# Kernel optimization log

Measured on AMD Instinct MI355X. Metric: run time of the kernel, lower is better.

The kernel has to match this reference:

```python
import jax, jax.numpy as jnp
import numpy as np
import math

B, N, D, H, A, OBS, NB = 256, 64, 512, 8, 64, 128, 4
HD = D // H
EPS = 1e-5


def layernorm(x, g, b):
    mu = jnp.mean(x, axis=-1, keepdims=True)
    var = jnp.mean((x - mu) ** 2, axis=-1, keepdims=True)
    return (x - mu) * jax.lax.rsqrt(var + EPS) * g + b


def gelu(x):
    return jax.nn.gelu(x, approximate=False)  # torch nn.GELU default = exact erf


def mha_masked(k_in, v_in, q_in, wq, wk, wv, wp, bq, bk, bv, bp):
    # weights stored [in, out]; torch Linear computes x @ W.T, same math with random init
    b, l, d = q_in.shape
    q = (q_in @ wq + bq).reshape(b, l, H, HD).transpose(0, 2, 1, 3)  # [B,H,L,hd]
    k = (k_in @ wk + bk).reshape(b, l, H, HD).transpose(0, 2, 1, 3)
    v = (v_in @ wv + bv).reshape(b, l, H, HD).transpose(0, 2, 1, 3)
    att = jnp.einsum('bhqd,bhkd->bhqk', q, k) * (1.0 / math.sqrt(HD))
    causal = jnp.tril(jnp.ones((l, l), dtype=bool))  # registered tril buffer in original MAT code
    att = jnp.where(causal[None, None], att, -jnp.inf)
    att = jax.nn.softmax(att, axis=-1)
    y = jnp.einsum('bhqk,bhkd->bhqd', att, v)
    y = y.transpose(0, 2, 1, 3).reshape(b, l, d)
    return y @ wp + bp


def setup_inputs() -> dict:
    key = jax.random.key(0)
    ks = iter(jax.random.split(key, 32))
    s = 0.02
    inp = {
        'action': jax.random.normal(next(ks), (B, N, A + 1), jnp.float32),
        'obs_rep': jax.random.normal(next(ks), (B, N, D), jnp.float32),
        'obs': jax.random.normal(next(ks), (B, N, OBS), jnp.float32),
        'w_ae': jax.random.normal(next(ks), (A + 1, D), jnp.float32) * s,
        'ln0_g': jnp.ones((D,), jnp.float32),
        'ln0_b': jnp.zeros((D,), jnp.float32),
        'blk_ln_g': jnp.ones((NB, 3, D), jnp.float32),
        'blk_ln_b': jnp.zeros((NB, 3, D), jnp.float32),
        'blk_wq': jax.random.normal(next(ks), (NB, 2, D, D), jnp.float32) * s,
        'blk_wk': jax.random.normal(next(ks), (NB, 2, D, D), jnp.float32) * s,
        'blk_wv': jax.random.normal(next(ks), (NB, 2, D, D), jnp.float32) * s,
        'blk_wp': jax.random.normal(next(ks), (NB, 2, D, D), jnp.float32) * s,
        'blk_bq': jnp.zeros((NB, 2, D), jnp.float32),
        'blk_bk': jnp.zeros((NB, 2, D), jnp.float32),
        'blk_bv': jnp.zeros((NB, 2, D), jnp.float32),
        'blk_bp': jnp.zeros((NB, 2, D), jnp.float32),
        'blk_w1': jax.random.normal(next(ks), (NB, D, D), jnp.float32) * s,
        'blk_b1': jnp.zeros((NB, D), jnp.float32),
        'blk_w2': jax.random.normal(next(ks), (NB, D, D), jnp.float32) * s,
        'blk_b2': jnp.zeros((NB, D), jnp.float32),
        'wh1': jax.random.normal(next(ks), (D, D), jnp.float32) * s,
        'bh1': jnp.zeros((D,), jnp.float32),
        'lnh_g': jnp.ones((D,), jnp.float32),
        'lnh_b': jnp.zeros((D,), jnp.float32),
        'wh2': jax.random.normal(next(ks), (D, A), jnp.float32) * s,
        'bh2': jnp.zeros((A,), jnp.float32),
    }
    return inp


def reference(action, obs_rep, obs, w_ae, ln0_g, ln0_b, blk_ln_g, blk_ln_b,
              blk_wq, blk_wk, blk_wv, blk_wp, blk_bq, blk_bk, blk_bv, blk_bp,
              blk_w1, blk_b1, blk_w2, blk_b2, wh1, bh1, lnh_g, lnh_b, wh2, bh2):
    # action encoder: Linear(no bias) + GELU, then LayerNorm
    x = layernorm(gelu(action @ w_ae), ln0_g, ln0_b)
    for i in range(NB):
        # sublayer 1: masked self-attn + residual + LN
        a1 = mha_masked(x, x, x, blk_wq[i, 0], blk_wk[i, 0], blk_wv[i, 0], blk_wp[i, 0],
                        blk_bq[i, 0], blk_bk[i, 0], blk_bv[i, 0], blk_bp[i, 0])
        x = layernorm(x + a1, blk_ln_g[i, 0], blk_ln_b[i, 0])
        # sublayer 2: masked cross-attn (key=x, value=x, query=obs_rep) + residual with obs_rep + LN
        a2 = mha_masked(x, x, obs_rep, blk_wq[i, 1], blk_wk[i, 1], blk_wv[i, 1], blk_wp[i, 1],
                        blk_bq[i, 1], blk_bk[i, 1], blk_bv[i, 1], blk_bp[i, 1])
        x = layernorm(obs_rep + a2, blk_ln_g[i, 1], blk_ln_b[i, 1])
        # sublayer 3: GELU MLP (D -> D -> D) + residual + LN
        m = gelu(x @ blk_w1[i] + blk_b1[i]) @ blk_w2[i] + blk_b2[i]
        x = layernorm(x + m, blk_ln_g[i, 2], blk_ln_b[i, 2])
    # head: Linear + GELU + LN + Linear
    h = layernorm(gelu(x @ wh1 + bh1), lnh_g, lnh_b)
    logit = h @ wh2 + bh2
    return logit
```

## Files before the change

kernel.cpp:

```cpp
#include <hip/hip_runtime.h>
#include <hip/hip_bf16.h>
#include <math.h>

namespace {

constexpr int B  = 256;
constexpr int N  = 64;
constexpr int D  = 512;
constexpr int H  = 8;
constexpr int NBLK = 4;
constexpr int M  = B * N;
constexpr float EPS = 1e-5f;
constexpr float SCALE = 0.125f;
constexpr int NEVER = 1 << 20;

typedef __attribute__((ext_vector_type(8))) short short8b;
typedef __attribute__((ext_vector_type(4))) float f32x4;

__device__ __forceinline__ float gelu_exact(float x) {
  return 0.5f * x * (1.0f + erff(x * 0.70710678118654752440f));
}

__device__ __forceinline__ unsigned short f2b_bits(float f) {
  __hip_bfloat16 h = __float2bfloat16(f);
  return *reinterpret_cast<unsigned short*>(&h);
}

#define GLOBAL_AS __attribute__((address_space(1)))
#define LDS_AS    __attribute__((address_space(3)))

__device__ __forceinline__ void gload_lds16(const void* g, void* l) {
  __builtin_amdgcn_global_load_lds((const GLOBAL_AS void*)g, (LDS_AS void*)l, 16, 0, 0);
}

template<bool GELU, int SPLIT>
__global__ __launch_bounds__(512, 2) void gemm_dp_kernel(
    const __hip_bfloat16* __restrict__ A,
    const __hip_bfloat16* __restrict__ Wt,
    const float* __restrict__ bias,
    __hip_bfloat16* __restrict__ out1, int ostr1,
    __hip_bfloat16* __restrict__ vt, int gy) {
  constexpr int K = 512;
  constexpr int NT = 8;
  __shared__ __hip_bfloat16 Als[3][128][64];
  __shared__ __hip_bfloat16 Bls[3][256][64];

  const int nwg = gridDim.x;
  const int hw  = blockIdx.x;
  const int cpx = nwg >> 3;
  const int lg  = (hw & 7) * cpx + (hw >> 3);
  const int bm  = (lg / gy) * 128;
  const int bn  = (lg % gy) * 256;

  const int tid  = threadIdx.x;
  const int wave = tid >> 6;
  const int lane = tid & 63;
  const int wm   = (wave >> 2) * 64;
  const int wn   = (wave & 3) * 64;
  const int fr   = lane & 15;
  const int fg   = lane >> 4;

  const int srow  = tid >> 3;
  const int sslot = (tid & 7) ^ (srow & 7);
  const __hip_bfloat16* gA = A  + (size_t)(bm + srow) * K + sslot * 8;
  const __hip_bfloat16* gB = Wt + (size_t)(bn + srow) * K + sslot * 8;

  auto STAGE = [&](int buf, int kt) {
    const int ko = kt * 64;
    char* la = (char*)&Als[buf][0][0] + wave * 1024;
    char* lb = (char*)&Bls[buf][0][0] + wave * 1024;
    gload_lds16(gA + ko,           la);
    gload_lds16(gA + 64 * K + ko,  la + 8192);
    gload_lds16(gB + ko,           lb);
    gload_lds16(gB + 64 * K + ko,  lb + 8192);
    gload_lds16(gB + 128 * K + ko, lb + 16384);
    gload_lds16(gB + 192 * K + ko, lb + 24576);
  };

  auto lda = [&](int buf, int mi, int ks) -> short8b {
    const int row  = wm + mi * 16 + fr;
    const int byte = row * 128 + (((ks << 2) | fg) ^ (fr & 7)) * 16;
    return *reinterpret_cast<const short8b*>((const char*)&Als[buf][0][0] + byte);
  };
  auto ldb = [&](int buf, int ni, int ks) -> short8b {
    const int row  = wn + ni * 16 + fr;
    const int byte = row * 128 + (((ks << 2) | fg) ^ (fr & 7)) * 16;
    return *reinterpret_cast<const short8b*>((const char*)&Bls[buf][0][0] + byte);
  };

  STAGE(0, 0);
  STAGE(1, 1);
  asm volatile("s_waitcnt vmcnt(6)" ::: "memory");
  __builtin_amdgcn_sched_barrier(0);
  __builtin_amdgcn_s_barrier();
  __builtin_amdgcn_sched_barrier(0);

  f32x4 acc[4][4] = {};
  for (int t = 0; t < NT; ++t) {
    const int cur = t % 3;
    if (t + 2 < NT) STAGE((t + 2) % 3, t + 2);

    short8b a0[4], b0[4], a1[4], b1[4];
#pragma unroll
    for (int mi = 0; mi < 4; ++mi) a0[mi] = lda(cur, mi, 0);
#pragma unroll
    for (int ni = 0; ni < 4; ++ni) b0[ni] = ldb(cur, ni, 0);
#pragma unroll
    for (int mi = 0; mi < 4; ++mi) a1[mi] = lda(cur, mi, 1);
#pragma unroll
    for (int ni = 0; ni < 4; ++ni) b1[ni] = ldb(cur, ni, 1);

    __builtin_amdgcn_s_setprio(1);
#pragma unroll
    for (int mi = 0; mi < 4; ++mi)
#pragma unroll
      for (int ni = 0; ni < 4; ++ni)
        acc[mi][ni] = __builtin_amdgcn_mfma_f32_16x16x32_bf16(a0[mi], b0[ni], acc[mi][ni], 0, 0, 0);
#pragma unroll
    for (int mi = 0; mi < 4; ++mi)
#pragma unroll
      for (int ni = 0; ni < 4; ++ni)
        acc[mi][ni] = __builtin_amdgcn_mfma_f32_16x16x32_bf16(a1[mi], b1[ni], acc[mi][ni], 0, 0, 0);
    __builtin_amdgcn_s_setprio(0);

    if (t + 2 < NT) {
      asm volatile("s_waitcnt vmcnt(6)" ::: "memory");
    } else {
      asm volatile("s_waitcnt vmcnt(0)" ::: "memory");
    }
    __builtin_amdgcn_sched_barrier(0);
    __builtin_amdgcn_s_barrier();
    __builtin_amdgcn_sched_barrier(0);
  }

#pragma unroll
  for (int ni = 0; ni < 4; ++ni) {
    const int col = bn + wn + ni * 16 + fr;
    const float bv = bias ? bias[col] : 0.f;
#pragma unroll
    for (int mi = 0; mi < 4; ++mi) {
      const int row0 = bm + wm + mi * 16 + fg * 4;
      if (col >= SPLIT) {
        const int vcol = col - SPLIT;
        ushort4 o;
        o.x = f2b_bits(acc[mi][ni][0] + bv);
        o.y = f2b_bits(acc[mi][ni][1] + bv);
        o.z = f2b_bits(acc[mi][ni][2] + bv);
        o.w = f2b_bits(acc[mi][ni][3] + bv);
        const int b8 = row0 >> 6, nl = row0 & 63;
        const int hh = vcol >> 6, dl = vcol & 63;
        *reinterpret_cast<ushort4*>(vt +
            ((size_t)(b8 * 8 + hh) * 4096 + dl * 64 + nl)) = o;
      } else {
#pragma unroll
        for (int q = 0; q < 4; ++q) {
          float v = acc[mi][ni][q] + bv;
          if (GELU) v = gelu_exact(v);
          out1[(size_t)(row0 + q) * ostr1 + col] = __float2bfloat16(v);
        }
      }
    }
  }
}

template<int KSTEPS, bool GELU, int SPLIT, bool F32OUT>
__global__ __launch_bounds__(256) void gemm_std_kernel(
    const __hip_bfloat16* __restrict__ A,
    const __hip_bfloat16* __restrict__ Wt,
    const float* __restrict__ bias,
    void* __restrict__ out1, int ostr1,
    __hip_bfloat16* __restrict__ vt, int nvalid) {
  constexpr int K = KSTEPS * 32;
  __shared__ __hip_bfloat16 Als[2][128][32];
  __shared__ __hip_bfloat16 Bls[2][128][32];

  const int bm   = blockIdx.x * 128;
  const int bn   = blockIdx.y * 128;
  const int tid  = threadIdx.x;
  const int wave = tid >> 6;
  const int lane = tid & 63;
  const int wm   = (wave >> 1) * 64;
  const int wn   = (wave & 1) * 64;
  const int fr   = lane & 15;
  const int fg   = lane >> 4;

  const int srow = (lane >> 2);
  const int scol = (lane & 3) * 8;
  const __hip_bfloat16* gA0 = A  + (size_t)(bm + wave * 32 + srow) * K + scol;
  const __hip_bfloat16* gA1 = gA0 + 16 * K;
  const __hip_bfloat16* gB0 = Wt + (size_t)(bn + wave * 32 + srow) * K + scol;
  const __hip_bfloat16* gB1 = gB0 + 16 * K;

  f32x4 acc[4][4] = {};

  auto stage = [&](int buf, int ks) {
    const int ko = ks * 32;
    gload_lds16(gA0 + ko, &Als[buf][wave * 32][0]);
    gload_lds16(gA1 + ko, &Als[buf][wave * 32 + 16][0]);
    gload_lds16(gB0 + ko, &Bls[buf][wave * 32][0]);
    gload_lds16(gB1 + ko, &Bls[buf][wave * 32 + 16][0]);
  };

  stage(0, 0);
  int buf = 0;
  for (int ks = 0; ks < KSTEPS; ++ks) {
    __syncthreads();
    if (ks + 1 < KSTEPS) stage(buf ^ 1, ks + 1);
    short8b a[4], b[4];
#pragma unroll
    for (int mi = 0; mi < 4; ++mi)
      a[mi] = *reinterpret_cast<const short8b*>(&Als[buf][wm + mi * 16 + fr][fg * 8]);
#pragma unroll
    for (int ni = 0; ni < 4; ++ni)
      b[ni] = *reinterpret_cast<const short8b*>(&Bls[buf][wn + ni * 16 + fr][fg * 8]);
#pragma unroll
    for (int mi = 0; mi < 4; ++mi)
#pragma unroll
      for (int ni = 0; ni < 4; ++ni)
        acc[mi][ni] = __builtin_amdgcn_mfma_f32_16x16x32_bf16(a[mi], b[ni], acc[mi][ni], 0, 0, 0);
    buf ^= 1;
  }

#pragma unroll
  for (int ni = 0; ni < 4; ++ni) {
    const int col = bn + wn + ni * 16 + fr;
    float bv = 0.f;
    if (bias) bv = (F32OUT && col >= nvalid) ? 0.f : bias[col];
#pragma unroll
    for (int mi = 0; mi < 4; ++mi) {
      const int row0 = bm + wm + mi * 16 + fg * 4;
      if (!F32OUT && col >= SPLIT) {
        const int vcol = col - SPLIT;
        ushort4 o;
        o.x = f2b_bits(acc[mi][ni][0] + bv);
        o.y = f2b_bits(acc[mi][ni][1] + bv);
        o.z = f2b_bits(acc[mi][ni][2] + bv);
        o.w = f2b_bits(acc[mi][ni][3] + bv);
        const int b8 = row0 >> 6, nl = row0 & 63;
        const int hh = vcol >> 6, dl = vcol & 63;
        *reinterpret_cast<ushort4*>(vt +
            ((size_t)(b8 * 8 + hh) * 4096 + dl * 64 + nl)) = o;
      } else {
#pragma unroll
        for (int q = 0; q < 4; ++q) {
          float v = acc[mi][ni][q] + bv;
          if (GELU) v = gelu_exact(v);
          if (F32OUT) {
            if (col < nvalid)
              ((float*)out1)[(size_t)(row0 + q) * ostr1 + col] = v;
          } else {
            ((__hip_bfloat16*)out1)[(size_t)(row0 + q) * ostr1 + col] = __float2bfloat16(v);
          }
        }
      }
    }
  }
}

template<int KSTEPS, bool GELU_PRE, bool RES>
__global__ __launch_bounds__(512) void gemm_ln_kernel(
    const __hip_bfloat16* __restrict__ A,
    const __hip_bfloat16* __restrict__ Wt,
    const float* __restrict__ bias,
    const float* __restrict__ res,
    const float* __restrict__ g, const float* __restrict__ bb,
    float* __restrict__ outF, __hip_bfloat16* __restrict__ outB) {
  constexpr int K = KSTEPS * 32;
  __shared__ __hip_bfloat16 Als[2][64][32];
  __shared__ __hip_bfloat16 Bls[2][512][32];
  __shared__ float red[64][8];
  __shared__ float mrow[64];
  __shared__ float rrow[64];

  const int bm   = blockIdx.x * 64;
  const int tid  = threadIdx.x;
  const int wave = tid >> 6;
  const int lane = tid & 63;
  const int fr   = lane & 15;
  const int fg   = lane >> 4;
  const int srow = lane >> 2;
  const int scol = (lane & 3) * 8;

  auto stage = [&](int buf, int ks) {
    const int ko = ks * 32;
    if (wave < 4)
      gload_lds16(A + (size_t)(bm + wave * 16 + srow) * K + ko + scol,
                  &Als[buf][wave * 16][0]);
#pragma unroll
    for (int c = 0; c < 4; ++c)
      gload_lds16(Wt + (size_t)(wave * 64 + c * 16 + srow) * K + ko + scol,
                  &Bls[buf][wave * 64 + c * 16][0]);
  };

  f32x4 acc[4][4] = {};
  stage(0, 0);
  int buf = 0;
  for (int ks = 0; ks < KSTEPS; ++ks) {
    __syncthreads();
    if (ks + 1 < KSTEPS) stage(buf ^ 1, ks + 1);
    short8b a[4], b[4];
#pragma unroll
    for (int mi = 0; mi < 4; ++mi)
      a[mi] = *reinterpret_cast<const short8b*>(&Als[buf][mi * 16 + fr][fg * 8]);
#pragma unroll
    for (int ni = 0; ni < 4; ++ni)
      b[ni] = *reinterpret_cast<const short8b*>(&Bls[buf][wave * 64 + ni * 16 + fr][fg * 8]);
#pragma unroll
    for (int mi = 0; mi < 4; ++mi)
#pragma unroll
      for (int ni = 0; ni < 4; ++ni)
        acc[mi][ni] = __builtin_amdgcn_mfma_f32_16x16x32_bf16(a[mi], b[ni], acc[mi][ni], 0, 0, 0);
    buf ^= 1;
  }

  float v[4][4][4];
  float bvc[4];
#pragma unroll
  for (int ni = 0; ni < 4; ++ni)
    bvc[ni] = bias ? bias[wave * 64 + ni * 16 + fr] : 0.f;
#pragma unroll
  for (int mi = 0; mi < 4; ++mi)
#pragma unroll
    for (int q = 0; q < 4; ++q) {
      const int row = bm + mi * 16 + fg * 4 + q;
#pragma unroll
      for (int ni = 0; ni < 4; ++ni) {
        float t = acc[mi][ni][q] + bvc[ni];
        if (GELU_PRE) t = gelu_exact(t);
        if (RES) t += res[(size_t)row * D + wave * 64 + ni * 16 + fr];
        v[mi][ni][q] = t;
      }
    }

  float ps[16];
#pragma unroll
  for (int mi = 0; mi < 4; ++mi)
#pragma unroll
    for (int q = 0; q < 4; ++q)
      ps[mi * 4 + q] = v[mi][0][q] + v[mi][1][q] + v[mi][2][q] + v[mi][3][q];
#pragma unroll
  for (int mask = 1; mask < 16; mask <<= 1)
#pragma unroll
    for (int t = 0; t < 16; ++t) ps[t] += __shfl_xor(ps[t], mask);
  if (fr == 0) {
#pragma unroll
    for (int mi = 0; mi < 4; ++mi)
#pragma unroll
      for (int q = 0; q < 4; ++q)
        red[mi * 16 + fg * 4 + q][wave] = ps[mi * 4 + q];
  }
  __syncthreads();
  if (tid < 64) {
    float s = 0.f;
#pragma unroll
    for (int w = 0; w < 8; ++w) s += red[tid][w];
    mrow[tid] = s * (1.f / 512.f);
  }
  __syncthreads();
  float mu[16];
#pragma unroll
  for (int mi = 0; mi < 4; ++mi)
#pragma unroll
    for (int q = 0; q < 4; ++q) mu[mi * 4 + q] = mrow[mi * 16 + fg * 4 + q];

  float ps2[16];
#pragma unroll
  for (int mi = 0; mi < 4; ++mi)
#pragma unroll
    for (int q = 0; q < 4; ++q) {
      const float m = mu[mi * 4 + q];
      float s = 0.f;
#pragma unroll
      for (int ni = 0; ni < 4; ++ni) {
        const float d = v[mi][ni][q] - m;
        s += d * d;
      }
      ps2[mi * 4 + q] = s;
    }
#pragma unroll
  for (int mask = 1; mask < 16; mask <<= 1)
#pragma unroll
    for (int t = 0; t < 16; ++t) ps2[t] += __shfl_xor(ps2[t], mask);
  if (fr == 0) {
#pragma unroll
    for (int mi = 0; mi < 4; ++mi)
#pragma unroll
      for (int q = 0; q < 4; ++q)
        red[mi * 16 + fg * 4 + q][wave] = ps2[mi * 4 + q];
  }
  __syncthreads();
  if (tid < 64) {
    float s = 0.f;
#pragma unroll
    for (int w = 0; w < 8; ++w) s += red[tid][w];
    rrow[tid] = rsqrtf(s * (1.f / 512.f) + EPS);
  }
  __syncthreads();

#pragma unroll
  for (int ni = 0; ni < 4; ++ni) {
    const int col = wave * 64 + ni * 16 + fr;
    const float gc = g[col], bc = bb[col];
#pragma unroll
    for (int mi = 0; mi < 4; ++mi)
#pragma unroll
      for (int q = 0; q < 4; ++q) {
        const int lrow = mi * 16 + fg * 4 + q;
        const int row = bm + lrow;
        const float o = (v[mi][ni][q] - mu[mi * 4 + q]) * rrow[lrow] * gc + bc;
        outF[(size_t)row * D + col] = o;
        outB[(size_t)row * D + col] = __float2bfloat16(o);
      }
  }
}

__global__ __launch_bounds__(256) void attn_mfma_kernel(
    const __hip_bfloat16* __restrict__ qg, int qstr,
    const __hip_bfloat16* __restrict__ kg, int kstr,
    const __hip_bfloat16* __restrict__ vt,
    __hip_bfloat16* __restrict__ yg) {
  __shared__ __align__(16) char smem[33280];
  unsigned short* Qs  = (unsigned short*)smem;
  unsigned short* Ks  = (unsigned short*)(smem + 8192);
  float*          Ss  = (float*)smem;
  unsigned short* Vts = (unsigned short*)(smem + 16896);
  unsigned short* Ps  = (unsigned short*)(smem + 25088);

  const int tid  = threadIdx.x;
  const int bh   = blockIdx.x;
  const int bidx = bh >> 3, h = bh & 7;
  const size_t rbase = (size_t)bidx * 64;
  const int col0 = h * 64;

  const __hip_bfloat16* vtg = vt + (size_t)bh * 4096;
#pragma unroll
  for (int p = 0; p < 2; ++p) {
    const int idx = tid + p * 256;
    const int row = idx >> 3, c8 = (idx & 7) * 8;
    const int lb  = (row * 128 + c8 * 2) ^ ((row & 7) << 4);
    const uint4 vq = *reinterpret_cast<const uint4*>(qg + (rbase + row) * qstr + col0 + c8);
    const uint4 vk = *reinterpret_cast<const uint4*>(kg + (rbase + row) * kstr + col0 + c8);
    const uint4 vv = *reinterpret_cast<const uint4*>(vtg + idx * 8);
    *reinterpret_cast<uint4*>((char*)Qs  + lb) = vq;
    *reinterpret_cast<uint4*>((char*)Ks  + lb) = vk;
    *reinterpret_cast<uint4*>((char*)Vts + lb) = vv;
  }
  __syncthreads();

  const int wave = tid >> 6, lane = tid & 63;
  const int fr = lane & 15, fg = lane >> 4;
  const int wr = (wave >> 1) * 32, wc = (wave & 1) * 32;

  auto ldfrag = [&](const unsigned short* base, int row, int ks) -> short8b {
    const int byte = (row * 128 + ks * 64 + fg * 16) ^ ((row & 7) << 4);
    return *reinterpret_cast<const short8b*>((const char*)base + byte);
  };

  f32x4 acc[2][2] = {};
#pragma unroll
  for (int ks = 0; ks < 2; ++ks) {
    short8b a[2], b[2];
    a[0] = ldfrag(Qs, wr + fr, ks);
    a[1] = ldfrag(Qs, wr + 16 + fr, ks);
    b[0] = ldfrag(Ks, wc + fr, ks);
    b[1] = ldfrag(Ks, wc + 16 + fr, ks);
#pragma unroll
    for (int mi = 0; mi < 2; ++mi)
#pragma unroll
      for (int ni = 0; ni < 2; ++ni)
        acc[mi][ni] = __builtin_amdgcn_mfma_f32_16x16x32_bf16(a[mi], b[ni], acc[mi][ni], 0, 0, 0);
  }
  __syncthreads();

#pragma unroll
  for (int mi = 0; mi < 2; ++mi)
#pragma unroll
    for (int ni = 0; ni < 2; ++ni) {
      const int m2 = wc + ni * 16 + fr;
#pragma unroll
      for (int r = 0; r < 4; ++r) {
        const int n = wr + mi * 16 + fg * 4 + r;
        Ss[n * 66 + m2] = (m2 <= n) ? acc[mi][ni][r] * SCALE : -1e30f;
      }
    }
  __syncthreads();

  for (int n = wave * 16; n < wave * 16 + 16; ++n) {
    const float vv = Ss[n * 66 + lane];
    float mx = vv;
#pragma unroll
    for (int off = 1; off < 64; off <<= 1) mx = fmaxf(mx, __shfl_xor(mx, off));
    const float p = (lane <= n) ? __expf(vv - mx) : 0.f;
    float sum = p;
#pragma unroll
    for (int off = 1; off < 64; off <<= 1) sum += __shfl_xor(sum, off);
    const int byte = (n * 128 + lane * 2) ^ ((n & 7) << 4);
    *(unsigned short*)((char*)Ps + byte) = f2b_bits(p / sum);
  }
  __syncthreads();

  f32x4 acc2[2][2] = {};
#pragma unroll
  for (int ks = 0; ks < 2; ++ks) {
    short8b a[2], b[2];
    a[0] = ldfrag(Ps, wr + fr, ks);
    a[1] = ldfrag(Ps, wr + 16 + fr, ks);
    b[0] = ldfrag(Vts, wc + fr, ks);
    b[1] = ldfrag(Vts, wc + 16 + fr, ks);
#pragma unroll
    for (int mi = 0; mi < 2; ++mi)
#pragma unroll
      for (int ni = 0; ni < 2; ++ni)
        acc2[mi][ni] = __builtin_amdgcn_mfma_f32_16x16x32_bf16(a[mi], b[ni], acc2[mi][ni], 0, 0, 0);
  }
#pragma unroll
  for (int mi = 0; mi < 2; ++mi)
#pragma unroll
    for (int r = 0; r < 4; ++r) {
      const int n = wr + mi * 16 + fg * 4 + r;
      yg[(rbase + n) * 512 + col0 + wc + fr]      = __float2bfloat16(acc2[mi][0][r]);
      yg[(rbase + n) * 512 + col0 + wc + 16 + fr] = __float2bfloat16(acc2[mi][1][r]);
    }
}

__global__ __launch_bounds__(256) void wconv_kernel(
    const float* __restrict__ src, __hip_bfloat16* __restrict__ dst,
    int soff, int sstr, long dstr) {
  __shared__ float tile[32][33];
  const int mat = blockIdx.z;
  const float* s = src + (size_t)(soff + mat * sstr) * D * D;
  __hip_bfloat16* d = dst + (size_t)mat * dstr;
  const int r0 = blockIdx.y * 32, c0 = blockIdx.x * 32;
  const int tr = threadIdx.x >> 5;
  const int tc = threadIdx.x & 31;
#pragma unroll
  for (int i = 0; i < 4; ++i)
    tile[tr + 8 * i][tc] = s[(size_t)(r0 + tr + 8 * i) * D + c0 + tc];
  __syncthreads();
#pragma unroll
  for (int i = 0; i < 4; ++i)
    d[(size_t)(c0 + tr + 8 * i) * D + r0 + tc] = __float2bfloat16(tile[tc][tr + 8 * i]);
}

__global__ __launch_bounds__(256) void cvt_kernel(
    const float* __restrict__ src, __hip_bfloat16* __restrict__ dst, int n4) {
  const int i = blockIdx.x * 256 + threadIdx.x;
  if (i < n4) {
    const float4 v = reinterpret_cast<const float4*>(src)[i];
    ushort4 o;
    o.x = f2b_bits(v.x); o.y = f2b_bits(v.y);
    o.z = f2b_bits(v.z); o.w = f2b_bits(v.w);
    reinterpret_cast<ushort4*>(dst)[i] = o;
  }
}

__global__ __launch_bounds__(256) void act_cvt_kernel(
    const float* __restrict__ src, __hip_bfloat16* __restrict__ dst) {
  for (int i = blockIdx.x * 256 + threadIdx.x; i < M * 96; i += gridDim.x * 256) {
    const int row = i / 96, k = i - row * 96;
    dst[i] = (k < 65) ? __float2bfloat16(src[(size_t)row * 65 + k]) : __float2bfloat16(0.f);
  }
}

__global__ __launch_bounds__(256) void wae_conv_kernel(
    const float* __restrict__ src, __hip_bfloat16* __restrict__ dst) {
  for (int i = blockIdx.x * 256 + threadIdx.x; i < 512 * 96; i += gridDim.x * 256) {
    const int n = i / 96, k = i - n * 96;
    dst[i] = (k < 65) ? __float2bfloat16(src[(size_t)k * 512 + n]) : __float2bfloat16(0.f);
  }
}

__global__ __launch_bounds__(256) void wh2_conv_kernel(
    const float* __restrict__ src, __hip_bfloat16* __restrict__ dst) {
  for (int i = blockIdx.x * 256 + threadIdx.x; i < 128 * 512; i += gridDim.x * 256) {
    const int n = i >> 9, k = i & 511;
    dst[i] = (n < 64) ? __float2bfloat16(src[(size_t)k * 64 + n]) : __float2bfloat16(0.f);
  }
}

__global__ __launch_bounds__(256) void pack_selfb_kernel(
    const float* __restrict__ bq, const float* __restrict__ bk,
    const float* __restrict__ bv, float* __restrict__ dst) {
  const int i = blockIdx.x * 256 + threadIdx.x;
  if (i < NBLK * 1536) {
    const int blk = i / 1536, c = i - blk * 1536;
    const int seg = c >> 9, cc = c & 511;
    const float* s = (seg == 0) ? bq : (seg == 1) ? bk : bv;
    dst[i] = s[(size_t)(blk * 2) * 512 + cc];
  }
}

__global__ __launch_bounds__(256) void pack_ckvb_kernel(
    const float* __restrict__ bk, const float* __restrict__ bv,
    float* __restrict__ dst) {
  const int i = blockIdx.x * 256 + threadIdx.x;
  if (i < NBLK * 1024) {
    const int blk = i >> 10, c = i & 1023;
    dst[i] = (c < 512) ? bk[(size_t)(blk * 2 + 1) * 512 + c]
                       : bv[(size_t)(blk * 2 + 1) * 512 + (c - 512)];
  }
}

}

extern "C" void kernel_launch(void* const* d_in, const int* in_sizes, int n_in,
                              void* d_out, int out_size, void* d_ws, size_t ws_size,
                              hipStream_t stream) {
  const float* action  = (const float*)d_in[0];
  const float* obs_rep = (const float*)d_in[1];
  const float* w_ae    = (const float*)d_in[3];
  const float* ln0_g   = (const float*)d_in[4];
  const float* ln0_b   = (const float*)d_in[5];
  const float* bln_g   = (const float*)d_in[6];
  const float* bln_b   = (const float*)d_in[7];
  const float* bwq     = (const float*)d_in[8];
  const float* bwk     = (const float*)d_in[9];
  const float* bwv     = (const float*)d_in[10];
  const float* bwp     = (const float*)d_in[11];
  const float* bbq     = (const float*)d_in[12];
  const float* bbk     = (const float*)d_in[13];
  const float* bbv     = (const float*)d_in[14];
  const float* bbp     = (const float*)d_in[15];
  const float* bw1     = (const float*)d_in[16];
  const float* bb1     = (const float*)d_in[17];
  const float* bw2     = (const float*)d_in[18];
  const float* bb2     = (const float*)d_in[19];
  const float* wh1     = (const float*)d_in[20];
  const float* bh1     = (const float*)d_in[21];
  const float* lnh_g   = (const float*)d_in[22];
  const float* lnh_b   = (const float*)d_in[23];
  const float* wh2     = (const float*)d_in[24];
  const float* bh2     = (const float*)d_in[25];

  char* ws = (char*)d_ws;
  const size_t MAT = (size_t)D * D;
  const size_t szF = (size_t)M * D * 4;
  const size_t szB = (size_t)M * D * 2;

  float* x            = (float*)ws;          ws += szF;
  __hip_bfloat16* xb  = (__hip_bfloat16*)ws; ws += szB;
  __hip_bfloat16* hb  = (__hip_bfloat16*)ws; ws += szB;
  __hip_bfloat16* vtb = (__hip_bfloat16*)ws; ws += szB;
  __hip_bfloat16* orb = (__hip_bfloat16*)ws; ws += szB;
  __hip_bfloat16* qkb = (__hip_bfloat16*)ws; ws += 2 * szB;
  __hip_bfloat16* qcb = (__hip_bfloat16*)ws; ws += szB;
  __hip_bfloat16* kb  = (__hip_bfloat16*)ws; ws += szB;
  __hip_bfloat16* actb = (__hip_bfloat16*)ws; ws += (size_t)M * 96 * 2;
  __hip_bfloat16* wSelf = (__hip_bfloat16*)ws; ws += (size_t)NBLK * 1536 * 512 * 2;
  __hip_bfloat16* wCq   = (__hip_bfloat16*)ws; ws += (size_t)NBLK * 512 * 512 * 2;
  __hip_bfloat16* wCkv  = (__hip_bfloat16*)ws; ws += (size_t)NBLK * 1024 * 512 * 2;
  __hip_bfloat16* wTp   = (__hip_bfloat16*)ws; ws += 8 * MAT * 2;
  __hip_bfloat16* wTw1  = (__hip_bfloat16*)ws; ws += 4 * MAT * 2;
  __hip_bfloat16* wTw2  = (__hip_bfloat16*)ws; ws += 4 * MAT * 2;
  __hip_bfloat16* wTh1  = (__hip_bfloat16*)ws; ws += MAT * 2;
  __hip_bfloat16* wh2p  = (__hip_bfloat16*)ws; ws += 128 * 512 * 2;
  __hip_bfloat16* waeT  = (__hip_bfloat16*)ws; ws += 512 * 96 * 2;
  float* selfb         = (float*)ws;         ws += (size_t)NBLK * 1536 * 4;
  float* ckvb          = (float*)ws;         ws += (size_t)NBLK * 1024 * 4;

  const long SS = 1536 * 512;
  wconv_kernel<<<dim3(16, 16, 4), 256, 0, stream>>>(bwq, wSelf, 0, 2, SS);
  wconv_kernel<<<dim3(16, 16, 4), 256, 0, stream>>>(bwk, wSelf + 512 * 512, 0, 2, SS);
  wconv_kernel<<<dim3(16, 16, 4), 256, 0, stream>>>(bwv, wSelf + 1024 * 512, 0, 2, SS);
  wconv_kernel<<<dim3(16, 16, 4), 256, 0, stream>>>(bwq, wCq, 1, 2, (long)MAT);
  wconv_kernel<<<dim3(16, 16, 4), 256, 0, stream>>>(bwk, wCkv, 1, 2, 1024 * 512L);
  wconv_kernel<<<dim3(16, 16, 4), 256, 0, stream>>>(bwv, wCkv + 512 * 512, 1, 2, 1024 * 512L);
  wconv_kernel<<<dim3(16, 16, 8), 256, 0, stream>>>(bwp, wTp, 0, 1, (long)MAT);
  wconv_kernel<<<dim3(16, 16, 4), 256, 0, stream>>>(bw1, wTw1, 0, 1, (long)MAT);
  wconv_kernel<<<dim3(16, 16, 4), 256, 0, stream>>>(bw2, wTw2, 0, 1, (long)MAT);
  wconv_kernel<<<dim3(16, 16, 1), 256, 0, stream>>>(wh1, wTh1, 0, 1, (long)MAT);
  wae_conv_kernel<<<192, 256, 0, stream>>>(w_ae, waeT);
  wh2_conv_kernel<<<256, 256, 0, stream>>>(wh2, wh2p);
  pack_selfb_kernel<<<(NBLK * 1536 + 255) / 256, 256, 0, stream>>>(bbq, bbk, bbv, selfb);
  pack_ckvb_kernel<<<(NBLK * 1024 + 255) / 256, 256, 0, stream>>>(bbk, bbv, ckvb);
  cvt_kernel<<<(M * D / 4 + 255) / 256, 256, 0, stream>>>(obs_rep, orb, M * D / 4);
  act_cvt_kernel<<<2048, 256, 0, stream>>>(action, actb);

  const int lnGrid = M / 64;

  gemm_ln_kernel<3, true, false><<<lnGrid, 512, 0, stream>>>(
      actb, waeT, nullptr, nullptr, ln0_g, ln0_b, x, xb);

  for (int i = 0; i < NBLK; ++i) {
    const float* g0 = bln_g + (size_t)(i * 3 + 0) * D;
    const float* b0 = bln_b + (size_t)(i * 3 + 0) * D;
    const float* g1 = bln_g + (size_t)(i * 3 + 1) * D;
    const float* b1 = bln_b + (size_t)(i * 3 + 1) * D;
    const float* g2 = bln_g + (size_t)(i * 3 + 2) * D;
    const float* b2 = bln_b + (size_t)(i * 3 + 2) * D;

    gemm_dp_kernel<false, 1024><<<M / 128 * 6, 512, 0, stream>>>(
        xb, wSelf + (size_t)i * SS, selfb + (size_t)i * 1536, qkb, 1024, vtb, 6);
    attn_mfma_kernel<<<B * H, 256, 0, stream>>>(qkb, 1024, qkb + 512, 1024, vtb, hb);
    gemm_ln_kernel<16, false, true><<<lnGrid, 512, 0, stream>>>(
        hb, wTp + (size_t)(i * 2) * MAT, bbp + (size_t)(i * 2) * D, x, g0, b0, x, xb);

    gemm_dp_kernel<false, NEVER><<<M / 128 * 2, 512, 0, stream>>>(
        orb, wCq + (size_t)i * MAT, bbq + (size_t)(i * 2 + 1) * D, qcb, 512, nullptr, 2);
    gemm_dp_kernel<false, 512><<<M / 128 * 4, 512, 0, stream>>>(
        xb, wCkv + (size_t)i * 1024 * 512, ckvb + (size_t)i * 1024, kb, 512, vtb, 4);
    attn_mfma_kernel<<<B * H, 256, 0, stream>>>(qcb, 512, kb, 512, vtb, hb);
    gemm_ln_kernel<16, false, true><<<lnGrid, 512, 0, stream>>>(
        hb, wTp + (size_t)(i * 2 + 1) * MAT, bbp + (size_t)(i * 2 + 1) * D,
        obs_rep, g1, b1, x, xb);

    gemm_dp_kernel<true, NEVER><<<M / 128 * 2, 512, 0, stream>>>(
        xb, wTw1 + (size_t)i * MAT, bb1 + (size_t)i * D, hb, 512, nullptr, 2);
    gemm_ln_kernel<16, false, true><<<lnGrid, 512, 0, stream>>>(
        hb, wTw2 + (size_t)i * MAT, bb2 + (size_t)i * D, x, g2, b2, x, xb);
  }

  gemm_ln_kernel<16, true, false><<<lnGrid, 512, 0, stream>>>(
      xb, wTh1, bh1, nullptr, lnh_g, lnh_b, x, xb);
  gemm_std_kernel<16, false, NEVER, true><<<dim3(M / 128, 1), 256, 0, stream>>>(
      xb, wh2p, bh2, (float*)d_out, 64, nullptr, 64);
}
```

Measured before the change: 1.139 ms.

## Keep the residual stream in bf16, batch the cross-attn Q projections, merge prep kernels

Drops the fp32 copy of the activation x. The LayerNorm-fused GEMMs now read the residual from the bf16 buffer and write only bf16 output, which cuts a large fp32 write and read from every sublayer. The four per-block cross-attention query projections of obs_rep are hoisted into one wide GEMM before the loop, since they do not depend on x. The many small weight-transpose and bias-packing launches are merged into two kernels. In exchange, the residual is rounded to bf16 at each step, which lowers numerical precision.

New measurement: 1.039 ms. 8.8% less time.

```diff
diff --git a/kernel.cpp b/kernel.cpp
--- a/kernel.cpp
+++ b/kernel.cpp
@@ -163,13 +163,12 @@
   }
 }
 
-template<int KSTEPS, bool GELU, int SPLIT, bool F32OUT>
-__global__ __launch_bounds__(256) void gemm_std_kernel(
+template<int KSTEPS>
+__global__ __launch_bounds__(256) void gemm_head_kernel(
     const __hip_bfloat16* __restrict__ A,
     const __hip_bfloat16* __restrict__ Wt,
     const float* __restrict__ bias,
-    void* __restrict__ out1, int ostr1,
-    __hip_bfloat16* __restrict__ vt, int nvalid) {
+    float* __restrict__ out1, int ostr1, int nvalid) {
   constexpr int K = KSTEPS * 32;
   __shared__ __hip_bfloat16 Als[2][128][32];
   __shared__ __hip_bfloat16 Bls[2][128][32];
@@ -224,35 +223,14 @@
 #pragma unroll
   for (int ni = 0; ni < 4; ++ni) {
     const int col = bn + wn + ni * 16 + fr;
-    float bv = 0.f;
-    if (bias) bv = (F32OUT && col >= nvalid) ? 0.f : bias[col];
+    if (col >= nvalid) continue;
+    const float bv = bias ? bias[col] : 0.f;
 #pragma unroll
     for (int mi = 0; mi < 4; ++mi) {
       const int row0 = bm + wm + mi * 16 + fg * 4;
-      if (!F32OUT && col >= SPLIT) {
-        const int vcol = col - SPLIT;
-        ushort4 o;
-        o.x = f2b_bits(acc[mi][ni][0] + bv);
-        o.y = f2b_bits(acc[mi][ni][1] + bv);
-        o.z = f2b_bits(acc[mi][ni][2] + bv);
-        o.w = f2b_bits(acc[mi][ni][3] + bv);
-        const int b8 = row0 >> 6, nl = row0 & 63;
-        const int hh = vcol >> 6, dl = vcol & 63;
-        *reinterpret_cast<ushort4*>(vt +
-            ((size_t)(b8 * 8 + hh) * 4096 + dl * 64 + nl)) = o;
-      } else {
-#pragma unroll
-        for (int q = 0; q < 4; ++q) {
-          float v = acc[mi][ni][q] + bv;
-          if (GELU) v = gelu_exact(v);
-          if (F32OUT) {
-            if (col < nvalid)
-              ((float*)out1)[(size_t)(row0 + q) * ostr1 + col] = v;
-          } else {
-            ((__hip_bfloat16*)out1)[(size_t)(row0 + q) * ostr1 + col] = __float2bfloat16(v);
-          }
-        }
-      }
+#pragma unroll
+      for (int q = 0; q < 4; ++q)
+        out1[(size_t)(row0 + q) * ostr1 + col] = acc[mi][ni][q] + bv;
     }
   }
 }
@@ -262,9 +240,9 @@
     const __hip_bfloat16* __restrict__ A,
     const __hip_bfloat16* __restrict__ Wt,
     const float* __restrict__ bias,
-    const float* __restrict__ res,
+    const __hip_bfloat16* __restrict__ resb,
     const float* __restrict__ g, const float* __restrict__ bb,
-    float* __restrict__ outF, __hip_bfloat16* __restrict__ outB) {
+    __hip_bfloat16* __restrict__ outB) {
   constexpr int K = KSTEPS * 32;
   __shared__ __hip_bfloat16 Als[2][64][32];
   __shared__ __hip_bfloat16 Bls[2][512][32];
@@ -327,7 +305,8 @@
       for (int ni = 0; ni < 4; ++ni) {
         float t = acc[mi][ni][q] + bvc[ni];
         if (GELU_PRE) t = gelu_exact(t);
-        if (RES) t += res[(size_t)row * D + wave * 64 + ni * 16 + fr];
+        if (RES)
+          t += __bfloat162float(resb[(size_t)row * D + wave * 64 + ni * 16 + fr]);
         v[mi][ni][q] = t;
       }
     }
@@ -408,7 +387,6 @@
         const int lrow = mi * 16 + fg * 4 + q;
         const int row = bm + lrow;
         const float o = (v[mi][ni][q] - mu[mi * 4 + q]) * rrow[lrow] * gc + bc;
-        outF[(size_t)row * D + col] = o;
         outB[(size_t)row * D + col] = __float2bfloat16(o);
       }
   }
@@ -523,23 +501,82 @@
     }
 }
 
-__global__ __launch_bounds__(256) void wconv_kernel(
-    const float* __restrict__ src, __hip_bfloat16* __restrict__ dst,
-    int soff, int sstr, long dstr) {
+__global__ __launch_bounds__(256) void wconv_all_kernel(
+    const float* __restrict__ bwq, const float* __restrict__ bwk,
+    const float* __restrict__ bwv, const float* __restrict__ bwp,
+    const float* __restrict__ bw1, const float* __restrict__ bw2,
+    const float* __restrict__ wh1,
+    __hip_bfloat16* __restrict__ wSelf, __hip_bfloat16* __restrict__ wCq,
+    __hip_bfloat16* __restrict__ wCkv, __hip_bfloat16* __restrict__ wTp,
+    __hip_bfloat16* __restrict__ wTw1, __hip_bfloat16* __restrict__ wTw2,
+    __hip_bfloat16* __restrict__ wTh1) {
+  const size_t MAT = (size_t)D * D;
+  const size_t SS = (size_t)1536 * 512, KV = (size_t)1024 * 512;
+  const int z = blockIdx.z;
+  const float* src;
+  __hip_bfloat16* dst;
+  if (z < 8)       { int i = z >> 1; src = bwq + (size_t)z * MAT;
+                     dst = (z & 1) ? wCq + (size_t)i * MAT : wSelf + (size_t)i * SS; }
+  else if (z < 16) { int zz = z - 8, i = zz >> 1; src = bwk + (size_t)zz * MAT;
+                     dst = (zz & 1) ? wCkv + (size_t)i * KV
+                                    : wSelf + (size_t)i * SS + 512 * 512; }
+  else if (z < 24) { int zz = z - 16, i = zz >> 1; src = bwv + (size_t)zz * MAT;
+                     dst = (zz & 1) ? wCkv + (size_t)i * KV + 512 * 512
+                                    : wSelf + (size_t)i * SS + 1024 * 512; }
+  else if (z < 32) { int zz = z - 24; src = bwp + (size_t)zz * MAT; dst = wTp + (size_t)zz * MAT; }
+  else if (z < 36) { int zz = z - 32; src = bw1 + (size_t)zz * MAT; dst = wTw1 + (size_t)zz * MAT; }
+  else if (z < 40) { int zz = z - 36; src = bw2 + (size_t)zz * MAT; dst = wTw2 + (size_t)zz * MAT; }
+  else             { src = wh1; dst = wTh1; }
+
   __shared__ float tile[32][33];
-  const int mat = blockIdx.z;
-  const float* s = src + (size_t)(soff + mat * sstr) * D * D;
-  __hip_bfloat16* d = dst + (size_t)mat * dstr;
   const int r0 = blockIdx.y * 32, c0 = blockIdx.x * 32;
   const int tr = threadIdx.x >> 5;
   const int tc = threadIdx.x & 31;
 #pragma unroll
   for (int i = 0; i < 4; ++i)
-    tile[tr + 8 * i][tc] = s[(size_t)(r0 + tr + 8 * i) * D + c0 + tc];
+    tile[tr + 8 * i][tc] = src[(size_t)(r0 + tr + 8 * i) * D + c0 + tc];
   __syncthreads();
 #pragma unroll
   for (int i = 0; i < 4; ++i)
-    d[(size_t)(c0 + tr + 8 * i) * D + r0 + tc] = __float2bfloat16(tile[tc][tr + 8 * i]);
+    dst[(size_t)(c0 + tr + 8 * i) * D + r0 + tc] = __float2bfloat16(tile[tc][tr + 8 * i]);
+}
+
+__global__ __launch_bounds__(256) void misc_prep_kernel(
+    const float* __restrict__ w_ae, const float* __restrict__ wh2,
+    const float* __restrict__ bbq, const float* __restrict__ bbk,
+    const float* __restrict__ bbv, const float* __restrict__ action,
+    __hip_bfloat16* __restrict__ waeT, __hip_bfloat16* __restrict__ wh2p,
+    float* __restrict__ selfb, float* __restrict__ ckvb,
+    float* __restrict__ bqc, __hip_bfloat16* __restrict__ actb) {
+  constexpr int R0 = 512 * 96, R1 = 128 * 512, R2 = NBLK * 1536,
+                R3 = NBLK * 1024, R4 = NBLK * 512, R5 = M * 96;
+  constexpr int total = R0 + R1 + R2 + R3 + R4 + R5;
+  for (int i = blockIdx.x * 256 + threadIdx.x; i < total; i += gridDim.x * 256) {
+    int j = i;
+    if (j < R0) {
+      const int n = j / 96, k = j - n * 96;
+      waeT[j] = (k < 65) ? __float2bfloat16(w_ae[(size_t)k * 512 + n]) : __float2bfloat16(0.f);
+    } else if ((j -= R0) < R1) {
+      const int n = j >> 9, k = j & 511;
+      wh2p[j] = (n < 64) ? __float2bfloat16(wh2[(size_t)k * 64 + n]) : __float2bfloat16(0.f);
+    } else if ((j -= R1) < R2) {
+      const int blk = j / 1536, c = j - blk * 1536;
+      const int seg = c >> 9, cc = c & 511;
+      const float* s = (seg == 0) ? bbq : (seg == 1) ? bbk : bbv;
+      selfb[j] = s[(size_t)(blk * 2) * 512 + cc];
+    } else if ((j -= R2) < R3) {
+      const int blk = j >> 10, c = j & 1023;
+      ckvb[j] = (c < 512) ? bbk[(size_t)(blk * 2 + 1) * 512 + c]
+                          : bbv[(size_t)(blk * 2 + 1) * 512 + (c - 512)];
+    } else if ((j -= R3) < R4) {
+      const int blk = j >> 9, c = j & 511;
+      bqc[j] = bbq[(size_t)(blk * 2 + 1) * 512 + c];
+    } else {
+      j -= R4;
+      const int row = j / 96, k = j - row * 96;
+      actb[j] = (k < 65) ? __float2bfloat16(action[(size_t)row * 65 + k]) : __float2bfloat16(0.f);
+    }
+  }
 }
 
 __global__ __launch_bounds__(256) void cvt_kernel(
@@ -551,53 +588,6 @@
     o.x = f2b_bits(v.x); o.y = f2b_bits(v.y);
     o.z = f2b_bits(v.z); o.w = f2b_bits(v.w);
     reinterpret_cast<ushort4*>(dst)[i] = o;
-  }
-}
-
-__global__ __launch_bounds__(256) void act_cvt_kernel(
-    const float* __restrict__ src, __hip_bfloat16* __restrict__ dst) {
-  for (int i = blockIdx.x * 256 + threadIdx.x; i < M * 96; i += gridDim.x * 256) {
-    const int row = i / 96, k = i - row * 96;
-    dst[i] = (k < 65) ? __float2bfloat16(src[(size_t)row * 65 + k]) : __float2bfloat16(0.f);
-  }
-}
-
-__global__ __launch_bounds__(256) void wae_conv_kernel(
-    const float* __restrict__ src, __hip_bfloat16* __restrict__ dst) {
-  for (int i = blockIdx.x * 256 + threadIdx.x; i < 512 * 96; i += gridDim.x * 256) {
-    const int n = i / 96, k = i - n * 96;
-    dst[i] = (k < 65) ? __float2bfloat16(src[(size_t)k * 512 + n]) : __float2bfloat16(0.f);
-  }
-}
-
-__global__ __launch_bounds__(256) void wh2_conv_kernel(
-    const float* __restrict__ src, __hip_bfloat16* __restrict__ dst) {
-  for (int i = blockIdx.x * 256 + threadIdx.x; i < 128 * 512; i += gridDim.x * 256) {
-    const int n = i >> 9, k = i & 511;
-    dst[i] = (n < 64) ? __float2bfloat16(src[(size_t)k * 64 + n]) : __float2bfloat16(0.f);
-  }
-}
-
-__global__ __launch_bounds__(256) void pack_selfb_kernel(
-    const float* __restrict__ bq, const float* __restrict__ bk,
-    const float* __restrict__ bv, float* __restrict__ dst) {
-  const int i = blockIdx.x * 256 + threadIdx.x;
-  if (i < NBLK * 1536) {
-    const int blk = i / 1536, c = i - blk * 1536;
-    const int seg = c >> 9, cc = c & 511;
-    const float* s = (seg == 0) ? bq : (seg == 1) ? bk : bv;
-    dst[i] = s[(size_t)(blk * 2) * 512 + cc];
-  }
-}
-
-__global__ __launch_bounds__(256) void pack_ckvb_kernel(
-    const float* __restrict__ bk, const float* __restrict__ bv,
-    float* __restrict__ dst) {
-  const int i = blockIdx.x * 256 + threadIdx.x;
-  if (i < NBLK * 1024) {
-    const int blk = i >> 10, c = i & 1023;
-    dst[i] = (c < 512) ? bk[(size_t)(blk * 2 + 1) * 512 + c]
-                       : bv[(size_t)(blk * 2 + 1) * 512 + (c - 512)];
   }
 }
 
@@ -634,16 +624,14 @@
 
   char* ws = (char*)d_ws;
   const size_t MAT = (size_t)D * D;
-  const size_t szF = (size_t)M * D * 4;
   const size_t szB = (size_t)M * D * 2;
 
-  float* x            = (float*)ws;          ws += szF;
   __hip_bfloat16* xb  = (__hip_bfloat16*)ws; ws += szB;
   __hip_bfloat16* hb  = (__hip_bfloat16*)ws; ws += szB;
   __hip_bfloat16* vtb = (__hip_bfloat16*)ws; ws += szB;
   __hip_bfloat16* orb = (__hip_bfloat16*)ws; ws += szB;
   __hip_bfloat16* qkb = (__hip_bfloat16*)ws; ws += 2 * szB;
-  __hip_bfloat16* qcb = (__hip_bfloat16*)ws; ws += szB;
+  __hip_bfloat16* qcb = (__hip_bfloat16*)ws; ws += 4 * szB;
   __hip_bfloat16* kb  = (__hip_bfloat16*)ws; ws += szB;
   __hip_bfloat16* actb = (__hip_bfloat16*)ws; ws += (size_t)M * 96 * 2;
   __hip_bfloat16* wSelf = (__hip_bfloat16*)ws; ws += (size_t)NBLK * 1536 * 512 * 2;
@@ -657,29 +645,24 @@
   __hip_bfloat16* waeT  = (__hip_bfloat16*)ws; ws += 512 * 96 * 2;
   float* selfb         = (float*)ws;         ws += (size_t)NBLK * 1536 * 4;
   float* ckvb          = (float*)ws;         ws += (size_t)NBLK * 1024 * 4;
-
-  const long SS = 1536 * 512;
-  wconv_kernel<<<dim3(16, 16, 4), 256, 0, stream>>>(bwq, wSelf, 0, 2, SS);
-  wconv_kernel<<<dim3(16, 16, 4), 256, 0, stream>>>(bwk, wSelf + 512 * 512, 0, 2, SS);
-  wconv_kernel<<<dim3(16, 16, 4), 256, 0, stream>>>(bwv, wSelf + 1024 * 512, 0, 2, SS);
-  wconv_kernel<<<dim3(16, 16, 4), 256, 0, stream>>>(bwq, wCq, 1, 2, (long)MAT);
-  wconv_kernel<<<dim3(16, 16, 4), 256, 0, stream>>>(bwk, wCkv, 1, 2, 1024 * 512L);
-  wconv_kernel<<<dim3(16, 16, 4), 256, 0, stream>>>(bwv, wCkv + 512 * 512, 1, 2, 1024 * 512L);
-  wconv_kernel<<<dim3(16, 16, 8), 256, 0, stream>>>(bwp, wTp, 0, 1, (long)MAT);
-  wconv_kernel<<<dim3(16, 16, 4), 256, 0, stream>>>(bw1, wTw1, 0, 1, (long)MAT);
-  wconv_kernel<<<dim3(16, 16, 4), 256, 0, stream>>>(bw2, wTw2, 0, 1, (long)MAT);
-  wconv_kernel<<<dim3(16, 16, 1), 256, 0, stream>>>(wh1, wTh1, 0, 1, (long)MAT);
-  wae_conv_kernel<<<192, 256, 0, stream>>>(w_ae, waeT);
-  wh2_conv_kernel<<<256, 256, 0, stream>>>(wh2, wh2p);
-  pack_selfb_kernel<<<(NBLK * 1536 + 255) / 256, 256, 0, stream>>>(bbq, bbk, bbv, selfb);
-  pack_ckvb_kernel<<<(NBLK * 1024 + 255) / 256, 256, 0, stream>>>(bbk, bbv, ckvb);
+  float* bqc           = (float*)ws;         ws += (size_t)NBLK * 512 * 4;
+
+  wconv_all_kernel<<<dim3(16, 16, 41), 256, 0, stream>>>(
+      bwq, bwk, bwv, bwp, bw1, bw2, wh1,
+      wSelf, wCq, wCkv, wTp, wTw1, wTw2, wTh1);
+  misc_prep_kernel<<<2048, 256, 0, stream>>>(
+      w_ae, wh2, bbq, bbk, bbv, action, waeT, wh2p, selfb, ckvb, bqc, actb);
   cvt_kernel<<<(M * D / 4 + 255) / 256, 256, 0, stream>>>(obs_rep, orb, M * D / 4);
-  act_cvt_kernel<<<2048, 256, 0, stream>>>(action, actb);
-
+
+  const size_t SS = (size_t)1536 * 512;
+  const size_t KV = (size_t)1024 * 512;
   const int lnGrid = M / 64;
 
   gemm_ln_kernel<3, true, false><<<lnGrid, 512, 0, stream>>>(
-      actb, waeT, nullptr, nullptr, ln0_g, ln0_b, x, xb);
+      actb, waeT, nullptr, nullptr, ln0_g, ln0_b, xb);
+
+  gemm_dp_kernel<false, NEVER><<<M / 128 * 8, 512, 0, stream>>>(
+      orb, wCq, bqc, qcb, 2048, nullptr, 8);
 
   for (int i = 0; i < NBLK; ++i) {
     const float* g0 = bln_g + (size_t)(i * 3 + 0) * D;
@@ -693,25 +676,24 @@
         xb, wSelf + (size_t)i * SS, selfb + (size_t)i * 1536, qkb, 1024, vtb, 6);
     attn_mfma_kernel<<<B * H, 256, 0, stream>>>(qkb, 1024, qkb + 512, 1024, vtb, hb);
     gemm_ln_kernel<16, false, true><<<lnGrid, 512, 0, stream>>>(
-        hb, wTp + (size_t)(i * 2) * MAT, bbp + (size_t)(i * 2) * D, x, g0, b0, x, xb);
-
-    gemm_dp_kernel<false, NEVER><<<M / 128 * 2, 512, 0, stream>>>(
-        orb, wCq + (size_t)i * MAT, bbq + (size_t)(i * 2 + 1) * D, qcb, 512, nullptr, 2);
+        hb, wTp + (size_t)(i * 2) * MAT, bbp + (size_t)(i * 2) * D, xb, g0, b0, xb);
+
     gemm_dp_kernel<false, 512><<<M / 128 * 4, 512, 0, stream>>>(
-        xb, wCkv + (size_t)i * 1024 * 512, ckvb + (size_t)i * 1024, kb, 512, vtb, 4);
-    attn_mfma_kernel<<<B * H, 256, 0, stream>>>(qcb, 512, kb, 512, vtb, hb);
+        xb, wCkv + (size_t)i * KV, ckvb + (size_t)i * 1024, kb, 512, vtb, 4);
+    attn_mfma_kernel<<<B * H, 256, 0, stream>>>(
+        qcb + (size_t)i * 512, 2048, kb, 512, vtb, hb);
     gemm_ln_kernel<16, false, true><<<lnGrid, 512, 0, stream>>>(
         hb, wTp + (size_t)(i * 2 + 1) * MAT, bbp + (size_t)(i * 2 + 1) * D,
-        obs_rep, g1, b1, x, xb);
+        orb, g1, b1, xb);
 
     gemm_dp_kernel<true, NEVER><<<M / 128 * 2, 512, 0, stream>>>(
         xb, wTw1 + (size_t)i * MAT, bb1 + (size_t)i * D, hb, 512, nullptr, 2);
     gemm_ln_kernel<16, false, true><<<lnGrid, 512, 0, stream>>>(
-        hb, wTw2 + (size_t)i * MAT, bb2 + (size_t)i * D, x, g2, b2, x, xb);
+        hb, wTw2 + (size_t)i * MAT, bb2 + (size_t)i * D, xb, g2, b2, xb);
   }
 
   gemm_ln_kernel<16, true, false><<<lnGrid, 512, 0, stream>>>(
-      xb, wTh1, bh1, nullptr, lnh_g, lnh_b, x, xb);
-  gemm_std_kernel<16, false, NEVER, true><<<dim3(M / 128, 1), 256, 0, stream>>>(
-      xb, wh2p, bh2, (float*)d_out, 64, nullptr, 64);
-}
+      xb, wTh1, bh1, nullptr, lnh_g, lnh_b, hb);
+  gemm_head_kernel<16><<<dim3(M / 128, 1), 256, 0, stream>>>(
+      hb, wh2p, bh2, (float*)d_out, 64, 64);
+}
```
